# Kernel tuning notes

Hardware: AMD Instinct MI355X
Metric: run time of the kernel (lower is better)

## Reference

```python
import jax, jax.numpy as jnp
import numpy as np

NUM_HEADS = 8
ATTN_BALANCE = 0.3
ROPE_THETA = 10000.0


def _mp_weight(w):
    # EDM2-style magnitude-preserving 1x1 conv weight: per-output-row normalize.
    # normalize(w) = w / (eps + ||w_row|| / sqrt(fan_in)); then divide by sqrt(fan_in)
    fan_in = w.shape[1]
    norm = jnp.linalg.norm(w, axis=1, keepdims=True)
    w_n = w / (1e-4 + norm / jnp.sqrt(jnp.asarray(fan_in, w.dtype)))
    return w_n / jnp.sqrt(jnp.asarray(fan_in, w.dtype))


def _rope(x, positions):
    # x: (b, m, t, hw, c). Rotate interleaved pairs along c; rotation angle depends
    # on the frame index (position), shared across spatial tokens within a frame.
    c = x.shape[-1]
    inv_freq = 1.0 / (ROPE_THETA ** (jnp.arange(0, c, 2, dtype=jnp.float32) / c))  # (c/2,)
    ang = positions.astype(jnp.float32)[:, None] * inv_freq[None, :]               # (t, c/2)
    cos = jnp.cos(ang)[None, None, :, None, :]
    sin = jnp.sin(ang)[None, None, :, None, :]
    x1, x2 = x[..., 0::2], x[..., 1::2]
    r1 = x1 * cos - x2 * sin
    r2 = x1 * sin + x2 * cos
    return jnp.stack([r1, r2], axis=-1).reshape(x.shape)


def _mp_sum(a, b, t):
    return (a * (1.0 - t) + b * t) / np.sqrt((1.0 - t) ** 2 + t ** 2)


def setup_inputs() -> dict:
    key = jax.random.key(0)
    ks = jax.random.split(key, 5)
    b, C, h, w = 4, 512, 16, 16
    m, T_cache = NUM_HEADS, 63
    c = C // m
    return {
        "x": jax.random.normal(ks[0], (b, C, h, w), jnp.float32),
        "cached_k": jax.random.normal(ks[1], (b, m, T_cache, h * w, c), jnp.float32),
        "cached_v": jax.random.normal(ks[2], (b, m, T_cache, h * w, c), jnp.float32),
        "w_qkv": jax.random.normal(ks[3], (3 * C, C), jnp.float32),
        "w_proj": jax.random.normal(ks[4], (C, C), jnp.float32),
    }


def reference(x, cached_k, cached_v, w_qkv, w_proj):
    # Inference path: one new frame per batch element, growing KV cache.
    b, C, h, w = x.shape
    m = NUM_HEADS
    c = C // m
    hw = h * w

    # qkv 1x1 MPConv: (b, 3C, h, w)
    y = jnp.einsum("bchw,oc->bohw", x, _mp_weight(w_qkv))
    # '(b t) (s m c) h w -> s b m t (hw) c' with t=1
    y = y.reshape(b, 3, m, c, hw).transpose(1, 0, 2, 4, 3)  # (3, b, m, hw, c)
    q = y[0][:, :, None]  # (b, m, 1, hw, c)
    k = y[1][:, :, None]
    v = y[2][:, :, None]

    # append to cache along frame dim
    k = jnp.concatenate([cached_k, k], axis=2)  # (b, m, T, hw, c)
    v = jnp.concatenate([cached_v, v], axis=2)
    T = k.shape[2]

    # RoPE over frame positions (query is the last frame)
    q = _rope(q, jnp.arange(T - 1, T))
    k = _rope(k, jnp.arange(T))

    # flatten frames into the KV sequence
    qf = q.reshape(b, m, hw, c)
    kf = k.reshape(b, m, T * hw, c)
    vf = v.reshape(b, m, T * hw, c)

    scores = jnp.einsum("bmqc,bmkc->bmqk", qf, kf) / np.sqrt(c)
    attn = jax.nn.softmax(scores, axis=-1)
    o = jnp.einsum("bmqk,bmkc->bmqc", attn, vf)  # (b, m, hw, c)

    # 'b m (t h w) c -> (b t) (c m) h w'  (channel index = c_idx * m + head)
    o = o.transpose(0, 3, 1, 2).reshape(b, C, h, w)

    o = jnp.einsum("bchw,oc->bohw", o, _mp_weight(w_proj))
    return _mp_sum(x, o, ATTN_BALANCE)
```

## Files before the change

### kernel.cpp

```cpp
#include <hip/hip_runtime.h>
#include <math.h>

#define HW 256
#define CDIM 64
#define NHEAD 8
#define CFULL 512
#define BATCH 4
#define TFRAMES 64
#define NKEY (TFRAMES*HW)
#define NSPLIT 8
#define KEYS_PER_SPLIT (NKEY/NSPLIT)
#define CHUNK 64
#define NCHUNK (KEYS_PER_SPLIT/CHUNK)

#define KLOG10K_64 0.14391156634543589f

#define KP 68
#define VP 72
#define PA 72

typedef _Float16 half4  __attribute__((ext_vector_type(4)));
typedef _Float16 half2v __attribute__((ext_vector_type(2)));
typedef float    floatx4 __attribute__((ext_vector_type(4)));

#define MFMA16(a,b,c) __builtin_amdgcn_mfma_f32_16x16x16f16((a),(b),(c),0,0,0)


__global__ void k_norm(const float* __restrict__ wqkv, const float* __restrict__ wproj,
                       _Float16* __restrict__ wq_h, _Float16* __restrict__ wp_h) {
    int row = blockIdx.x;
    int t = threadIdx.x;
    float a, b;
    const float* src;
    if (row < 1536) {
        src = wqkv + row*CFULL;
        a = src[t]; b = src[t+256];
    } else {
        src = wproj + (row-1536)*CFULL;
        int ic1 = (t & 63)*8 + (t >> 6);
        int k2 = t + 256;
        int ic2 = (k2 & 63)*8 + (k2 >> 6);
        a = src[ic1]; b = src[ic2];
    }
    float v = a*a + b*b;
    #pragma unroll
    for (int o = 32; o >= 1; o >>= 1) v += __shfl_down(v, o, 64);
    __shared__ float red[4];
    if ((t & 63) == 0) red[t >> 6] = v;
    __syncthreads();
    float ss = red[0] + red[1] + red[2] + red[3];
    float norm = sqrtf(ss);
    const float s512 = 22.627416997969522f;
    float scale = 1.0f / ((1e-4f + norm / s512) * s512);
    if (row < 1536) {
        wq_h[row*CFULL + t]       = (_Float16)(a*scale);
        wq_h[row*CFULL + t + 256] = (_Float16)(b*scale);
    } else {
        int r2 = row - 1536;
        wp_h[r2*CFULL + t]       = (_Float16)(a*scale);
        wp_h[r2*CFULL + t + 256] = (_Float16)(b*scale);
    }
}

__global__ void k_xT(const float* __restrict__ x, _Float16* __restrict__ xt_h) {
    int pb = blockIdx.x;
    int cb = blockIdx.y;
    int b  = blockIdx.z;
    int t  = threadIdx.x;
    int p  = pb*64 + (t & 63);
    int c0 = cb*64 + (t >> 6)*16;
    half4 h[4];
    #pragma unroll
    for (int j = 0; j < 16; j++) {
        float val = x[((long)(b*CFULL + c0 + j))*HW + p];
        h[j >> 2][j & 3] = (_Float16)val;
    }
    _Float16* dst = xt_h + ((long)(b*HW + p))*CFULL + c0;
    #pragma unroll
    for (int j = 0; j < 4; j++) *(half4*)(dst + j*4) = h[j];
}

__global__ __launch_bounds__(256) void k_gemm_qkv(
        const _Float16* __restrict__ wq_h, const _Float16* __restrict__ xt_h,
        float* __restrict__ q, float* __restrict__ kn, float* __restrict__ vn) {
    int bx = blockIdx.x;
    int by = blockIdx.y;
    int b  = blockIdx.z;
    int t  = threadIdx.x;
    int wave = t >> 6, lane = t & 63, ln = lane & 15, quad = lane >> 4;
    __shared__ _Float16 As[64*PA];
    __shared__ _Float16 Bs[64*PA];
    int obase = bx*64, pbase = by*64;
    int lrow = t >> 2, lseg = t & 3;
    const _Float16* ag = wq_h + (long)(obase + lrow)*CFULL + lseg*16;
    const _Float16* bg = xt_h + (long)(b*HW + pbase + lrow)*CFULL + lseg*16;
    uint4 ar0 = *(const uint4*)ag,     ar1 = *(const uint4*)(ag + 8);
    uint4 br0 = *(const uint4*)bg,     br1 = *(const uint4*)(bg + 8);
    floatx4 acc[4];
    #pragma unroll
    for (int nt = 0; nt < 4; nt++) acc[nt] = (floatx4){0.f,0.f,0.f,0.f};
    for (int kc = 0; kc < 8; kc++) {
        __syncthreads();
        *(uint4*)&As[lrow*PA + lseg*16]     = ar0;
        *(uint4*)&As[lrow*PA + lseg*16 + 8] = ar1;
        *(uint4*)&Bs[lrow*PA + lseg*16]     = br0;
        *(uint4*)&Bs[lrow*PA + lseg*16 + 8] = br1;
        __syncthreads();
        if (kc < 7) {
            const _Float16* an = ag + (kc+1)*64;
            const _Float16* bn = bg + (kc+1)*64;
            ar0 = *(const uint4*)an; ar1 = *(const uint4*)(an + 8);
            br0 = *(const uint4*)bn; br1 = *(const uint4*)(bn + 8);
        }
        #pragma unroll
        for (int ks = 0; ks < 4; ks++) {
            half4 af = *(const half4*)&As[(wave*16 + ln)*PA + ks*16 + quad*4];
            #pragma unroll
            for (int nt = 0; nt < 4; nt++) {
                half4 bf = *(const half4*)&Bs[(nt*16 + ln)*PA + ks*16 + quad*4];
                acc[nt] = MFMA16(af, bf, acc[nt]);
            }
        }
    }
    int sec  = obase >> 9;
    int head = (obase >> 6) & 7;
    int bm   = b*NHEAD + head;
    int ch0  = wave*16 + quad*4;
    if (sec == 2) {
        #pragma unroll
        for (int nt = 0; nt < 4; nt++) {
            int p = pbase + nt*16 + ln;
            float4 o4; o4.x = acc[nt][0]; o4.y = acc[nt][1]; o4.z = acc[nt][2]; o4.w = acc[nt][3];
            *(float4*)&vn[((long)(bm*HW + p))*CDIM + ch0] = o4;
        }
    } else {
        float* dst = (sec == 0) ? q : kn;
        float fr0 = __expf(-(float)ch0       * KLOG10K_64);
        float fr1 = __expf(-(float)(ch0 + 2) * KLOG10K_64);
        float s0, c0, s1, c1;
        __sincosf(63.0f*fr0, &s0, &c0);
        __sincosf(63.0f*fr1, &s1, &c1);
        #pragma unroll
        for (int nt = 0; nt < 4; nt++) {
            int p = pbase + nt*16 + ln;
            float4 o4;
            o4.x = acc[nt][0]*c0 - acc[nt][1]*s0;
            o4.y = acc[nt][0]*s0 + acc[nt][1]*c0;
            o4.z = acc[nt][2]*c1 - acc[nt][3]*s1;
            o4.w = acc[nt][2]*s1 + acc[nt][3]*c1;
            *(float4*)&dst[((long)(bm*HW + p))*CDIM + ch0] = o4;
        }
    }
}

__global__ __launch_bounds__(512, 1) void k_attn(
        const float* __restrict__ q, const float* __restrict__ kc, const float* __restrict__ vc,
        const float* __restrict__ kn, const float* __restrict__ vn,
        float* __restrict__ o_part, float* __restrict__ ml) {
    const int bm = blockIdx.x;
    const int s  = blockIdx.y;
    const int t  = threadIdx.x;
    const int wave = t >> 6;
    const int lane = t & 63;
    const int ln   = lane & 15;
    const int quad = lane >> 4;
    const int qbase = wave * 32;

    __shared__ _Float16 Ks[CHUNK*KP];
    __shared__ _Float16 Vt[CDIM*VP];

    half4 qf[2][4];
    #pragma unroll
    for (int qt = 0; qt < 2; qt++)
        #pragma unroll
        for (int ks = 0; ks < 4; ks++) {
            const float* qp = q + ((long)(bm*HW + qbase + qt*16 + ln))*CDIM + ks*16 + quad*4;
            float4 f = *(const float4*)qp;
            half4 h;
            h[0] = (_Float16)(f.x*0.125f); h[1] = (_Float16)(f.y*0.125f);
            h[2] = (_Float16)(f.z*0.125f); h[3] = (_Float16)(f.w*0.125f);
            qf[qt][ks] = h;
        }

    floatx4 oacc[4][2];
    #pragma unroll
    for (int ct = 0; ct < 4; ct++)
        #pragma unroll
        for (int qt = 0; qt < 2; qt++)
            oacc[ct][qt] = (floatx4){0.f,0.f,0.f,0.f};
    float m_[2] = {-1e30f, -1e30f};
    float l_[2] = {0.f, 0.f};

    for (int chunk = 0; chunk < NCHUNK; chunk++) {
        int g0   = s*KEYS_PER_SPLIT + chunk*CHUNK;
        int tfr  = g0 >> 8;
        int poff = g0 & 255;
        const float *ksrc, *vsrc;
        bool rope;
        if (tfr < 63) {
            long base = ((long)((bm*63 + tfr)*HW + poff)) * CDIM;
            ksrc = kc + base; vsrc = vc + base; rope = true;
        } else {
            long base = ((long)(bm*HW + poff)) * CDIM;
            ksrc = kn + base; vsrc = vn + base; rope = false;
        }
        float tpos = (float)tfr;
        __syncthreads();
        #pragma unroll
        for (int it = 0; it < 2; it++) {
            int i   = t + it*512;
            int key = i >> 4;
            int ch  = (i & 15) * 4;
            float4 f = *(const float4*)(ksrc + key*CDIM + ch);
            if (rope) {
                float fr0 = __expf(-(float)ch       * KLOG10K_64);
                float fr1 = __expf(-(float)(ch + 2) * KLOG10K_64);
                float s0, c0, s1, c1;
                __sincosf(tpos*fr0, &s0, &c0);
                __sincosf(tpos*fr1, &s1, &c1);
                float4 r;
                r.x = f.x*c0 - f.y*s0;
                r.y = f.x*s0 + f.y*c0;
                r.z = f.z*c1 - f.w*s1;
                r.w = f.z*s1 + f.w*c1;
                f = r;
            }
            half4 h;
            h[0]=(_Float16)f.x; h[1]=(_Float16)f.y; h[2]=(_Float16)f.z; h[3]=(_Float16)f.w;
            *(half4*)&Ks[key*KP + ch] = h;
        }
        {
            int kp = t & 31;
            int ch = (t >> 5) * 4;
            float4 a = *(const float4*)(vsrc + (2*kp  )*CDIM + ch);
            float4 b = *(const float4*)(vsrc + (2*kp+1)*CDIM + ch);
            float av[4] = {a.x,a.y,a.z,a.w};
            float bv[4] = {b.x,b.y,b.z,b.w};
            #pragma unroll
            for (int i = 0; i < 4; i++) {
                half2v h; h[0] = (_Float16)av[i]; h[1] = (_Float16)bv[i];
                *(half2v*)&Vt[(ch+i)*VP + 2*kp] = h;
            }
        }
        __syncthreads();

        floatx4 sacc[4][2];
        #pragma unroll
        for (int kt = 0; kt < 4; kt++)
            #pragma unroll
            for (int qt = 0; qt < 2; qt++)
                sacc[kt][qt] = (floatx4){0.f,0.f,0.f,0.f};
        #pragma unroll
        for (int ks = 0; ks < 4; ks++) {
            half4 kf[4];
            #pragma unroll
            for (int kt = 0; kt < 4; kt++)
                kf[kt] = *(const half4*)&Ks[(kt*16 + ln)*KP + ks*16 + quad*4];
            #pragma unroll
            for (int kt = 0; kt < 4; kt++)
                #pragma unroll
                for (int qt = 0; qt < 2; qt++)
                    sacc[kt][qt] = MFMA16(kf[kt], qf[qt][ks], sacc[kt][qt]);
        }

        half4 ptf[4][2];
        #pragma unroll
        for (int qt = 0; qt < 2; qt++) {
            float tmax = -1e30f;
            #pragma unroll
            for (int kt = 0; kt < 4; kt++)
                #pragma unroll
                for (int r = 0; r < 4; r++)
                    tmax = fmaxf(tmax, sacc[kt][qt][r]);
            tmax = fmaxf(tmax, __shfl_xor(tmax, 16, 64));
            tmax = fmaxf(tmax, __shfl_xor(tmax, 32, 64));
            float mnew  = fmaxf(m_[qt], tmax);
            float alpha = __expf(m_[qt] - mnew);
            float lsum = 0.f;
            #pragma unroll
            for (int kt = 0; kt < 4; kt++) {
                half4 ph;
                #pragma unroll
                for (int r = 0; r < 4; r++) {
                    float p = __expf(sacc[kt][qt][r] - mnew);
                    lsum += p;
                    ph[r] = (_Float16)p;
                }
                ptf[kt][qt] = ph;
            }
            lsum += __shfl_xor(lsum, 16, 64);
            lsum += __shfl_xor(lsum, 32, 64);
            l_[qt] = l_[qt]*alpha + lsum;
            m_[qt] = mnew;
            #pragma unroll
            for (int ct = 0; ct < 4; ct++)
                #pragma unroll
                for (int r = 0; r < 4; r++)
                    oacc[ct][qt][r] *= alpha;
        }

        #pragma unroll
        for (int kt = 0; kt < 4; kt++) {
            half4 vf[4];
            #pragma unroll
            for (int ct = 0; ct < 4; ct++)
                vf[ct] = *(const half4*)&Vt[(ct*16 + ln)*VP + kt*16 + quad*4];
            #pragma unroll
            for (int ct = 0; ct < 4; ct++)
                #pragma unroll
                for (int qt = 0; qt < 2; qt++)
                    oacc[ct][qt] = MFMA16(vf[ct], ptf[kt][qt], oacc[ct][qt]);
        }
    }

    long ob = ((long)(bm*NSPLIT + s)) * CDIM * HW;
    #pragma unroll
    for (int ct = 0; ct < 4; ct++)
        #pragma unroll
        for (int qt = 0; qt < 2; qt++)
            #pragma unroll
            for (int r = 0; r < 4; r++)
                o_part[ob + (long)(ct*16 + quad*4 + r)*HW + qbase + qt*16 + ln] = oacc[ct][qt][r];
    long mb = ((long)(bm*NSPLIT + s)) * 2 * HW;
    if (quad == 0) {
        #pragma unroll
        for (int qt = 0; qt < 2; qt++) {
            int qq = qbase + qt*16 + ln;
            ml[mb + qq]      = m_[qt];
            ml[mb + HW + qq] = l_[qt];
        }
    }
}

__global__ void k_combine(const float* __restrict__ o_part, const float* __restrict__ ml,
                          _Float16* __restrict__ omt_h) {
    int bm  = blockIdx.x;
    int chg = blockIdx.y;
    int p   = threadIdx.x;
    float ms[NSPLIT], ls[NSPLIT];
    float mmax = -1e30f;
    #pragma unroll
    for (int s2 = 0; s2 < NSPLIT; s2++) {
        long mb = ((long)(bm*NSPLIT + s2)) * 2 * HW;
        ms[s2] = ml[mb + p];
        ls[s2] = ml[mb + HW + p];
        mmax = fmaxf(mmax, ms[s2]);
    }
    float wgt[NSPLIT];
    float wsum = 0.f;
    #pragma unroll
    for (int s2 = 0; s2 < NSPLIT; s2++) { wgt[s2] = __expf(ms[s2]-mmax); wsum += wgt[s2]*ls[s2]; }
    float inv = 1.0f / wsum;
    float acc[16];
    #pragma unroll
    for (int i = 0; i < 16; i++) acc[i] = 0.f;
    #pragma unroll
    for (int s2 = 0; s2 < NSPLIT; s2++) {
        float w = wgt[s2];
        const float* src = o_part + (((long)(bm*NSPLIT + s2))*CDIM + chg*16)*HW + p;
        #pragma unroll
        for (int i = 0; i < 16; i++) acc[i] += w * src[(long)i*HW];
    }
    int b = bm >> 3, head = bm & 7;
    _Float16* dst = omt_h + ((long)(b*HW + p))*CFULL + head*64 + chg*16;
    half4 h[4];
    #pragma unroll
    for (int i = 0; i < 16; i++) h[i >> 2][i & 3] = (_Float16)(acc[i]*inv);
    #pragma unroll
    for (int j = 0; j < 4; j++) *(half4*)(dst + j*4) = h[j];
}

__global__ __launch_bounds__(256) void k_gemm_proj(
        const _Float16* __restrict__ wp_h, const _Float16* __restrict__ omt_h,
        const float* __restrict__ x, float* __restrict__ out) {
    int bx = blockIdx.x;
    int by = blockIdx.y;
    int b  = blockIdx.z;
    int t  = threadIdx.x;
    int wave = t >> 6, lane = t & 63, ln = lane & 15, quad = lane >> 4;
    __shared__ _Float16 As[64*PA];
    __shared__ _Float16 Bs[64*PA];
    int obase = bx*64, pbase = by*64;
    int lrow = t >> 2, lseg = t & 3;
    const _Float16* ag = wp_h  + (long)(obase + lrow)*CFULL + lseg*16;
    const _Float16* bg = omt_h + (long)(b*HW + pbase + lrow)*CFULL + lseg*16;
    uint4 ar0 = *(const uint4*)ag, ar1 = *(const uint4*)(ag + 8);
    uint4 br0 = *(const uint4*)bg, br1 = *(const uint4*)(bg + 8);
    floatx4 acc[4];
    #pragma unroll
    for (int nt = 0; nt < 4; nt++) acc[nt] = (floatx4){0.f,0.f,0.f,0.f};
    for (int kc = 0; kc < 8; kc++) {
        __syncthreads();
        *(uint4*)&As[lrow*PA + lseg*16]     = ar0;
        *(uint4*)&As[lrow*PA + lseg*16 + 8] = ar1;
        *(uint4*)&Bs[lrow*PA + lseg*16]     = br0;
        *(uint4*)&Bs[lrow*PA + lseg*16 + 8] = br1;
        __syncthreads();
        if (kc < 7) {
            const _Float16* an = ag + (kc+1)*64;
            const _Float16* bn = bg + (kc+1)*64;
            ar0 = *(const uint4*)an; ar1 = *(const uint4*)(an + 8);
            br0 = *(const uint4*)bn; br1 = *(const uint4*)(bn + 8);
        }
        #pragma unroll
        for (int ks = 0; ks < 4; ks++) {
            half4 af = *(const half4*)&As[(wave*16 + ln)*PA + ks*16 + quad*4];
            #pragma unroll
            for (int nt = 0; nt < 4; nt++) {
                half4 bf = *(const half4*)&Bs[(nt*16 + ln)*PA + ks*16 + quad*4];
                acc[nt] = MFMA16(af, bf, acc[nt]);
            }
        }
    }
    const float inv_mp = 1.3130643285972254f;
    int o0 = obase + wave*16 + quad*4;
    #pragma unroll
    for (int nt = 0; nt < 4; nt++) {
        int p = pbase + nt*16 + ln;
        #pragma unroll
        for (int r = 0; r < 4; r++) {
            long idx = ((long)(b*CFULL + o0 + r))*HW + p;
            out[idx] = (x[idx]*0.7f + acc[nt][r]*0.3f) * inv_mp;
        }
    }
}

extern "C" void kernel_launch(void* const* d_in, const int* in_sizes, int n_in,
                              void* d_out, int out_size, void* d_ws, size_t ws_size,
                              hipStream_t stream) {
    const float* x     = (const float*)d_in[0];
    const float* kc    = (const float*)d_in[1];
    const float* vc    = (const float*)d_in[2];
    const float* wqkv  = (const float*)d_in[3];
    const float* wproj = (const float*)d_in[4];
    float* out = (float*)d_out;
    float* ws  = (float*)d_ws;

    _Float16* wq_h  = (_Float16*)ws;
    _Float16* wp_h  = (_Float16*)(ws + 393216);
    _Float16* xt_h  = (_Float16*)(ws + 524288);
    float* q        = ws + 786432;
    float* kn       = ws + 1310720;
    float* vn       = ws + 1835008;
    float* o_part   = ws + 2359296;
    float* ml       = ws + 6553600;
    _Float16* omt_h = (_Float16*)(ws + 6684672);

    hipLaunchKernelGGL(k_norm,      dim3(2048),    dim3(256), 0, stream, wqkv, wproj, wq_h, wp_h);
    hipLaunchKernelGGL(k_xT,        dim3(4,8,4),   dim3(256), 0, stream, x, xt_h);
    hipLaunchKernelGGL(k_gemm_qkv,  dim3(24,4,4),  dim3(256), 0, stream, wq_h, xt_h, q, kn, vn);
    hipLaunchKernelGGL(k_attn,      dim3(32,8),    dim3(512), 0, stream, q, kc, vc, kn, vn, o_part, ml);
    hipLaunchKernelGGL(k_combine,   dim3(32,4),    dim3(256), 0, stream, o_part, ml, omt_h);
    hipLaunchKernelGGL(k_gemm_proj, dim3(8,4,4),   dim3(256), 0, stream, wp_h, omt_h, x, out);
}
```

Baseline: 348.1 us.

## Double-buffer attention KV tiles, double splits, fp16 partials, merge prep kernels

The attention kernel now uses double-buffered LDS for K/V tiles, with register prefetch of the next chunk issued during compute so global load latency overlaps the MFMA work. The split count rises from 8 to 16 and the launch-bounds occupancy hint changes to 4 to put more blocks in flight. Partial outputs are stored as fp16, which halves combine traffic but adds rounding error before the split merge. The weight-normalization and x-transpose kernels are fused into one launch, and the w_proj permutation moves from the load side to the store side. The combine kernel is regridded to 4 channels per block.

```diff
diff --git a/kernel.cpp b/kernel.cpp
--- a/kernel.cpp
+++ b/kernel.cpp
@@ -8,7 +8,7 @@
 #define BATCH 4
 #define TFRAMES 64
 #define NKEY (TFRAMES*HW)
-#define NSPLIT 8
+#define NSPLIT 16
 #define KEYS_PER_SPLIT (NKEY/NSPLIT)
 #define CHUNK 64
 #define NCHUNK (KEYS_PER_SPLIT/CHUNK)
@@ -26,58 +26,50 @@
 #define MFMA16(a,b,c) __builtin_amdgcn_mfma_f32_16x16x16f16((a),(b),(c),0,0,0)
 
 
-__global__ void k_norm(const float* __restrict__ wqkv, const float* __restrict__ wproj,
-                       _Float16* __restrict__ wq_h, _Float16* __restrict__ wp_h) {
-    int row = blockIdx.x;
+__global__ void k_prep(const float* __restrict__ wqkv, const float* __restrict__ wproj,
+                       const float* __restrict__ x,
+                       _Float16* __restrict__ wq_h, _Float16* __restrict__ wp_h,
+                       _Float16* __restrict__ xt_h) {
+    int bid = blockIdx.x;
     int t = threadIdx.x;
-    float a, b;
-    const float* src;
-    if (row < 1536) {
-        src = wqkv + row*CFULL;
-        a = src[t]; b = src[t+256];
+    if (bid < 2048) {
+        int row = bid;
+        const float* src = (row < 1536) ? wqkv + row*CFULL : wproj + (row-1536)*CFULL;
+        float a = src[t], b = src[t+256];
+        float v = a*a + b*b;
+        #pragma unroll
+        for (int o = 32; o >= 1; o >>= 1) v += __shfl_down(v, o, 64);
+        __shared__ float red[4];
+        if ((t & 63) == 0) red[t >> 6] = v;
+        __syncthreads();
+        float ss = red[0] + red[1] + red[2] + red[3];
+        float norm = sqrtf(ss);
+        const float s512 = 22.627416997969522f;
+        float scale = 1.0f / ((1e-4f + norm / s512) * s512);
+        if (row < 1536) {
+            wq_h[row*CFULL + t]       = (_Float16)(a*scale);
+            wq_h[row*CFULL + t + 256] = (_Float16)(b*scale);
+        } else {
+            int r2 = row - 1536;
+            int kp_ = (t & 7)*64 + (t >> 3);
+            wp_h[r2*CFULL + kp_]      = (_Float16)(a*scale);
+            wp_h[r2*CFULL + kp_ + 32] = (_Float16)(b*scale);
+        }
     } else {
-        src = wproj + (row-1536)*CFULL;
-        int ic1 = (t & 63)*8 + (t >> 6);
-        int k2 = t + 256;
-        int ic2 = (k2 & 63)*8 + (k2 >> 6);
-        a = src[ic1]; b = src[ic2];
-    }
-    float v = a*a + b*b;
-    #pragma unroll
-    for (int o = 32; o >= 1; o >>= 1) v += __shfl_down(v, o, 64);
-    __shared__ float red[4];
-    if ((t & 63) == 0) red[t >> 6] = v;
-    __syncthreads();
-    float ss = red[0] + red[1] + red[2] + red[3];
-    float norm = sqrtf(ss);
-    const float s512 = 22.627416997969522f;
-    float scale = 1.0f / ((1e-4f + norm / s512) * s512);
-    if (row < 1536) {
-        wq_h[row*CFULL + t]       = (_Float16)(a*scale);
-        wq_h[row*CFULL + t + 256] = (_Float16)(b*scale);
-    } else {
-        int r2 = row - 1536;
-        wp_h[r2*CFULL + t]       = (_Float16)(a*scale);
-        wp_h[r2*CFULL + t + 256] = (_Float16)(b*scale);
-    }
-}
-
-__global__ void k_xT(const float* __restrict__ x, _Float16* __restrict__ xt_h) {
-    int pb = blockIdx.x;
-    int cb = blockIdx.y;
-    int b  = blockIdx.z;
-    int t  = threadIdx.x;
-    int p  = pb*64 + (t & 63);
-    int c0 = cb*64 + (t >> 6)*16;
-    half4 h[4];
-    #pragma unroll
-    for (int j = 0; j < 16; j++) {
-        float val = x[((long)(b*CFULL + c0 + j))*HW + p];
-        h[j >> 2][j & 3] = (_Float16)val;
-    }
-    _Float16* dst = xt_h + ((long)(b*HW + p))*CFULL + c0;
-    #pragma unroll
-    for (int j = 0; j < 4; j++) *(half4*)(dst + j*4) = h[j];
+        int xb = bid - 2048;
+        int pb = xb & 3, cb = (xb >> 2) & 7, b = xb >> 5;
+        int p  = pb*64 + (t & 63);
+        int c0 = cb*64 + (t >> 6)*16;
+        half4 h[4];
+        #pragma unroll
+        for (int j = 0; j < 16; j++) {
+            float val = x[((long)(b*CFULL + c0 + j))*HW + p];
+            h[j >> 2][j & 3] = (_Float16)val;
+        }
+        _Float16* dst = xt_h + ((long)(b*HW + p))*CFULL + c0;
+        #pragma unroll
+        for (int j = 0; j < 4; j++) *(half4*)(dst + j*4) = h[j];
+    }
 }
 
 __global__ __launch_bounds__(256) void k_gemm_qkv(
@@ -153,10 +145,10 @@
     }
 }
 
-__global__ __launch_bounds__(512, 1) void k_attn(
+__global__ __launch_bounds__(512, 4) void k_attn(
         const float* __restrict__ q, const float* __restrict__ kc, const float* __restrict__ vc,
         const float* __restrict__ kn, const float* __restrict__ vn,
-        float* __restrict__ o_part, float* __restrict__ ml) {
+        _Float16* __restrict__ o_part, float* __restrict__ ml) {
     const int bm = blockIdx.x;
     const int s  = blockIdx.y;
     const int t  = threadIdx.x;
@@ -166,8 +158,8 @@
     const int quad = lane >> 4;
     const int qbase = wave * 32;
 
-    __shared__ _Float16 Ks[CHUNK*KP];
-    __shared__ _Float16 Vt[CDIM*VP];
+    __shared__ _Float16 Ks[2][CHUNK*KP];
+    __shared__ _Float16 Vt[2][CDIM*VP];
 
     half4 qf[2][4];
     #pragma unroll
@@ -191,57 +183,69 @@
     float m_[2] = {-1e30f, -1e30f};
     float l_[2] = {0.f, 0.f};
 
-    for (int chunk = 0; chunk < NCHUNK; chunk++) {
-        int g0   = s*KEYS_PER_SPLIT + chunk*CHUNK;
-        int tfr  = g0 >> 8;
-        int poff = g0 & 255;
+    const int key0 = t >> 4;
+    const int chk  = (t & 15) * 4;
+    const int kp   = t & 31;
+    const int chv  = (t >> 5) * 4;
+    const float fr0 = __expf(-(float)chk       * KLOG10K_64);
+    const float fr1 = __expf(-(float)(chk + 2) * KLOG10K_64);
+
+    float4 ka, kb, va, vb;
+
+    auto prefetch = [&](int c) -> int {
+        int g0 = s*KEYS_PER_SPLIT + c*CHUNK;
+        int tfr = g0 >> 8, poff = g0 & 255;
         const float *ksrc, *vsrc;
-        bool rope;
         if (tfr < 63) {
-            long base = ((long)((bm*63 + tfr)*HW + poff)) * CDIM;
-            ksrc = kc + base; vsrc = vc + base; rope = true;
+            long base = ((long)((bm*63 + tfr)*HW + poff))*CDIM;
+            ksrc = kc + base; vsrc = vc + base;
         } else {
-            long base = ((long)(bm*HW + poff)) * CDIM;
-            ksrc = kn + base; vsrc = vn + base; rope = false;
-        }
-        float tpos = (float)tfr;
-        __syncthreads();
-        #pragma unroll
-        for (int it = 0; it < 2; it++) {
-            int i   = t + it*512;
-            int key = i >> 4;
-            int ch  = (i & 15) * 4;
-            float4 f = *(const float4*)(ksrc + key*CDIM + ch);
-            if (rope) {
-                float fr0 = __expf(-(float)ch       * KLOG10K_64);
-                float fr1 = __expf(-(float)(ch + 2) * KLOG10K_64);
-                float s0, c0, s1, c1;
-                __sincosf(tpos*fr0, &s0, &c0);
-                __sincosf(tpos*fr1, &s1, &c1);
-                float4 r;
-                r.x = f.x*c0 - f.y*s0;
-                r.y = f.x*s0 + f.y*c0;
-                r.z = f.z*c1 - f.w*s1;
-                r.w = f.z*s1 + f.w*c1;
-                f = r;
-            }
-            half4 h;
-            h[0]=(_Float16)f.x; h[1]=(_Float16)f.y; h[2]=(_Float16)f.z; h[3]=(_Float16)f.w;
-            *(half4*)&Ks[key*KP + ch] = h;
-        }
-        {
-            int kp = t & 31;
-            int ch = (t >> 5) * 4;
-            float4 a = *(const float4*)(vsrc + (2*kp  )*CDIM + ch);
-            float4 b = *(const float4*)(vsrc + (2*kp+1)*CDIM + ch);
-            float av[4] = {a.x,a.y,a.z,a.w};
-            float bv[4] = {b.x,b.y,b.z,b.w};
-            #pragma unroll
-            for (int i = 0; i < 4; i++) {
-                half2v h; h[0] = (_Float16)av[i]; h[1] = (_Float16)bv[i];
-                *(half2v*)&Vt[(ch+i)*VP + 2*kp] = h;
-            }
-        }
+            long base = ((long)(bm*HW + poff))*CDIM;
+            ksrc = kn + base; vsrc = vn + base;
+        }
+        ka = *(const float4*)(ksrc + key0*CDIM + chk);
+        kb = *(const float4*)(ksrc + (key0+32)*CDIM + chk);
+        va = *(const float4*)(vsrc + (2*kp  )*CDIM + chv);
+        vb = *(const float4*)(vsrc + (2*kp+1)*CDIM + chv);
+        return tfr;
+    };
+
+    auto write_buf = [&](int d, int tfr) {
+        float4 fka = ka, fkb = kb;
+        if (tfr < 63) {
+            float tp = (float)tfr;
+            float s0, c0, s1, c1;
+            __sincosf(tp*fr0, &s0, &c0);
+            __sincosf(tp*fr1, &s1, &c1);
+            float4 r;
+            r.x = fka.x*c0 - fka.y*s0; r.y = fka.x*s0 + fka.y*c0;
+            r.z = fka.z*c1 - fka.w*s1; r.w = fka.z*s1 + fka.w*c1;
+            fka = r;
+            r.x = fkb.x*c0 - fkb.y*s0; r.y = fkb.x*s0 + fkb.y*c0;
+            r.z = fkb.z*c1 - fkb.w*s1; r.w = fkb.z*s1 + fkb.w*c1;
+            fkb = r;
+        }
+        half4 h;
+        h[0]=(_Float16)fka.x; h[1]=(_Float16)fka.y; h[2]=(_Float16)fka.z; h[3]=(_Float16)fka.w;
+        *(half4*)&Ks[d][key0*KP + chk] = h;
+        h[0]=(_Float16)fkb.x; h[1]=(_Float16)fkb.y; h[2]=(_Float16)fkb.z; h[3]=(_Float16)fkb.w;
+        *(half4*)&Ks[d][(key0+32)*KP + chk] = h;
+        float av[4] = {va.x,va.y,va.z,va.w};
+        float bv[4] = {vb.x,vb.y,vb.z,vb.w};
+        #pragma unroll
+        for (int i = 0; i < 4; i++) {
+            half2v hv; hv[0] = (_Float16)av[i]; hv[1] = (_Float16)bv[i];
+            *(half2v*)&Vt[d][(chv+i)*VP + 2*kp] = hv;
+        }
+    };
+
+    int tfr0 = prefetch(0);
+    write_buf(0, tfr0);
+    int tfr_next = 0;
+
+    for (int c = 0; c < NCHUNK; c++) {
+        const int buf = c & 1;
+        if (c+1 < NCHUNK) tfr_next = prefetch(c+1);
         __syncthreads();
 
         floatx4 sacc[4][2];
@@ -255,7 +259,7 @@
             half4 kf[4];
             #pragma unroll
             for (int kt = 0; kt < 4; kt++)
-                kf[kt] = *(const half4*)&Ks[(kt*16 + ln)*KP + ks*16 + quad*4];
+                kf[kt] = *(const half4*)&Ks[buf][(kt*16 + ln)*KP + ks*16 + quad*4];
             #pragma unroll
             for (int kt = 0; kt < 4; kt++)
                 #pragma unroll
@@ -304,13 +308,15 @@
             half4 vf[4];
             #pragma unroll
             for (int ct = 0; ct < 4; ct++)
-                vf[ct] = *(const half4*)&Vt[(ct*16 + ln)*VP + kt*16 + quad*4];
+                vf[ct] = *(const half4*)&Vt[buf][(ct*16 + ln)*VP + kt*16 + quad*4];
             #pragma unroll
             for (int ct = 0; ct < 4; ct++)
                 #pragma unroll
                 for (int qt = 0; qt < 2; qt++)
                     oacc[ct][qt] = MFMA16(vf[ct], ptf[kt][qt], oacc[ct][qt]);
         }
+
+        if (c+1 < NCHUNK) write_buf((c+1) & 1, tfr_next);
     }
 
     long ob = ((long)(bm*NSPLIT + s)) * CDIM * HW;
@@ -320,7 +326,8 @@
         for (int qt = 0; qt < 2; qt++)
             #pragma unroll
             for (int r = 0; r < 4; r++)
-                o_part[ob + (long)(ct*16 + quad*4 + r)*HW + qbase + qt*16 + ln] = oacc[ct][qt][r];
+                o_part[ob + (long)(ct*16 + quad*4 + r)*HW + qbase + qt*16 + ln] =
+                    (_Float16)oacc[ct][qt][r];
     long mb = ((long)(bm*NSPLIT + s)) * 2 * HW;
     if (quad == 0) {
         #pragma unroll
@@ -332,7 +339,7 @@
     }
 }
 
-__global__ void k_combine(const float* __restrict__ o_part, const float* __restrict__ ml,
+__global__ void k_combine(const _Float16* __restrict__ o_part, const float* __restrict__ ml,
                           _Float16* __restrict__ omt_h) {
     int bm  = blockIdx.x;
     int chg = blockIdx.y;
@@ -351,23 +358,19 @@
     #pragma unroll
     for (int s2 = 0; s2 < NSPLIT; s2++) { wgt[s2] = __expf(ms[s2]-mmax); wsum += wgt[s2]*ls[s2]; }
     float inv = 1.0f / wsum;
-    float acc[16];
-    #pragma unroll
-    for (int i = 0; i < 16; i++) acc[i] = 0.f;
+    float acc[4] = {0.f, 0.f, 0.f, 0.f};
     #pragma unroll
     for (int s2 = 0; s2 < NSPLIT; s2++) {
         float w = wgt[s2];
-        const float* src = o_part + (((long)(bm*NSPLIT + s2))*CDIM + chg*16)*HW + p;
-        #pragma unroll
-        for (int i = 0; i < 16; i++) acc[i] += w * src[(long)i*HW];
+        const _Float16* src = o_part + (((long)(bm*NSPLIT + s2))*CDIM + chg*4)*HW + p;
+        #pragma unroll
+        for (int i = 0; i < 4; i++) acc[i] += w * (float)src[(long)i*HW];
     }
     int b = bm >> 3, head = bm & 7;
-    _Float16* dst = omt_h + ((long)(b*HW + p))*CFULL + head*64 + chg*16;
-    half4 h[4];
-    #pragma unroll
-    for (int i = 0; i < 16; i++) h[i >> 2][i & 3] = (_Float16)(acc[i]*inv);
-    #pragma unroll
-    for (int j = 0; j < 4; j++) *(half4*)(dst + j*4) = h[j];
+    half4 h;
+    #pragma unroll
+    for (int i = 0; i < 4; i++) h[i] = (_Float16)(acc[i]*inv);
+    *(half4*)(omt_h + ((long)(b*HW + p))*CFULL + head*64 + chg*4) = h;
 }
 
 __global__ __launch_bounds__(256) void k_gemm_proj(
@@ -442,14 +445,13 @@
     float* q        = ws + 786432;
     float* kn       = ws + 1310720;
     float* vn       = ws + 1835008;
-    float* o_part   = ws + 2359296;
+    _Float16* o_part= (_Float16*)(ws + 2359296);
     float* ml       = ws + 6553600;
-    _Float16* omt_h = (_Float16*)(ws + 6684672);
-
-    hipLaunchKernelGGL(k_norm,      dim3(2048),    dim3(256), 0, stream, wqkv, wproj, wq_h, wp_h);
-    hipLaunchKernelGGL(k_xT,        dim3(4,8,4),   dim3(256), 0, stream, x, xt_h);
-    hipLaunchKernelGGL(k_gemm_qkv,  dim3(24,4,4),  dim3(256), 0, stream, wq_h, xt_h, q, kn, vn);
-    hipLaunchKernelGGL(k_attn,      dim3(32,8),    dim3(512), 0, stream, q, kc, vc, kn, vn, o_part, ml);
-    hipLaunchKernelGGL(k_combine,   dim3(32,4),    dim3(256), 0, stream, o_part, ml, omt_h);
-    hipLaunchKernelGGL(k_gemm_proj, dim3(8,4,4),   dim3(256), 0, stream, wp_h, omt_h, x, out);
-}
+    _Float16* omt_h = (_Float16*)(ws + 6815744);
+
+    hipLaunchKernelGGL(k_prep,      dim3(2176),       dim3(256), 0, stream, wqkv, wproj, x, wq_h, wp_h, xt_h);
+    hipLaunchKernelGGL(k_gemm_qkv,  dim3(24,4,4),     dim3(256), 0, stream, wq_h, xt_h, q, kn, vn);
+    hipLaunchKernelGGL(k_attn,      dim3(32,NSPLIT),  dim3(512), 0, stream, q, kc, vc, kn, vn, o_part, ml);
+    hipLaunchKernelGGL(k_combine,   dim3(32,16),      dim3(256), 0, stream, o_part, ml, omt_h);
+    hipLaunchKernelGGL(k_gemm_proj, dim3(8,4,4),      dim3(256), 0, stream, wp_h, omt_h, x, out);
+}
```

Measured after the change: 404.9 us. +16.3%, slower.
